# Kernel tuning notes

Measured on AMD Instinct MI355X. Metric: run time of the kernel, lower is better.

The kernel has to match this reference:

```python
import jax, jax.numpy as jnp
import numpy as np

# Config mirroring init_kwargs
B, N, DM = 16, 512, 512          # batch, max_ast_len, hidden_size
PAR_HEADS, BRO_HEADS = 4, 4
H = PAR_HEADS + BRO_HEADS        # 8 heads
DK = DM // H                     # 64
R = 8                            # max_rel_pos
L = 2                            # num_layers
DFF = 4 * DM
EPS = 1e-5


def setup_inputs() -> dict:
    key = jax.random.key(0)
    ks = jax.random.split(key, 24)
    s = 0.02
    inp = {
        "src_emb": jax.random.normal(ks[0], (B, N, DM), jnp.float32),
        "par_edges": jax.random.randint(ks[1], (B, R, N), 0, N, jnp.int32),
        "bro_edges": jax.random.randint(ks[2], (B, R, N), 0, N, jnp.int32),
        # relative-position embedding tables (par heads ++ bro heads along head axis,
        # exactly what concat_vec(rel_par_*, rel_bro_*, dim=1) produces): [H, R, DK]
        "rel_q": s * jax.random.normal(ks[3], (H, R, DK), jnp.float32),
        "rel_k": s * jax.random.normal(ks[4], (H, R, DK), jnp.float32),
        "rel_v": s * jax.random.normal(ks[5], (H, R, DK), jnp.float32),
        # per-layer weights, stacked over layers
        "Wq": s * jax.random.normal(ks[6], (L, DM, DM), jnp.float32),
        "Wk": s * jax.random.normal(ks[7], (L, DM, DM), jnp.float32),
        "Wv": s * jax.random.normal(ks[8], (L, DM, DM), jnp.float32),
        "Wo": s * jax.random.normal(ks[9], (L, DM, DM), jnp.float32),
        "ln1_g": jnp.ones((L, DM), jnp.float32),
        "ln1_b": jnp.zeros((L, DM), jnp.float32),
        "W1": s * jax.random.normal(ks[10], (L, DM, DFF), jnp.float32),
        "b1": jnp.zeros((L, DFF), jnp.float32),
        "W2": s * jax.random.normal(ks[11], (L, DFF, DM), jnp.float32),
        "b2": jnp.zeros((L, DM), jnp.float32),
        "ln2_g": jnp.ones((L, DM), jnp.float32),
        "ln2_b": jnp.zeros((L, DM), jnp.float32),
        "normf_g": jnp.ones((DM,), jnp.float32),
        "normf_b": jnp.zeros((DM,), jnp.float32),
    }
    return inp


def _ln(x, g, b):
    m = x.mean(-1, keepdims=True)
    v = ((x - m) ** 2).mean(-1, keepdims=True)
    return (x - m) * jax.lax.rsqrt(v + EPS) * g + b


def _gather_nodes(t, idx):
    # t: [B,H,N,DK], idx: [B,H,R,N,1] -> [B,H,R,N,DK] gathered along node axis
    t_b = jnp.broadcast_to(t[:, :, None], (B, H, R, N, DK))
    return jnp.take_along_axis(t_b, idx, axis=3)


def _forward(src_emb, rel_q, rel_k, rel_v, Wq, Wk, Wv, Wo, ln1_g, ln1_b,
             W1, b1, W2, b2, ln2_g, ln2_b, normf_g, normf_b,
             par_edges, bro_edges):
    # start_nodes = concat_pos: repeat par edges over par heads, bro over bro heads
    start = jnp.concatenate(
        [jnp.repeat(par_edges[:, None], PAR_HEADS, axis=1),
         jnp.repeat(bro_edges[:, None], BRO_HEADS, axis=1)], axis=1)  # [B,H,R,N]
    idx = start[..., None].astype(jnp.int32)  # [B,H,R,N,1]
    scale = 1.0 / np.sqrt(DK)
    x = src_emb
    for i in range(L):
        q = (x @ Wq[i]).reshape(B, N, H, DK).transpose(0, 2, 1, 3)  # bhnd
        k = (x @ Wk[i]).reshape(B, N, H, DK).transpose(0, 2, 1, 3)
        v = (x @ Wv[i]).reshape(B, N, H, DK).transpose(0, 2, 1, 3)
        k_s = _gather_nodes(k, idx)  # [B,H,R,N,DK]
        v_s = _gather_nodes(v, idx)
        # Shaw-style relational scores over the R sparse neighbors only
        scores = (jnp.einsum('bhnd,bhrnd->bhrn', q, k_s)
                  + jnp.einsum('bhnd,hrd->bhrn', q, rel_k)
                  + jnp.einsum('hrd,bhrnd->bhrn', rel_q, k_s)) * scale
        attn = jax.nn.softmax(scores, axis=2)  # softmax over relative positions
        ctx = (jnp.einsum('bhrn,bhrnd->bhnd', attn, v_s)
               + jnp.einsum('bhrn,hrd->bhnd', attn, rel_v))
        ctx = ctx.transpose(0, 2, 1, 3).reshape(B, N, DM)
        x = _ln(x + ctx @ Wo[i], ln1_g[i], ln1_b[i])
        ff = jax.nn.relu(x @ W1[i] + b1[i]) @ W2[i] + b2[i]
        x = _ln(x + ff, ln2_g[i], ln2_b[i])
    return _ln(x, normf_g, normf_b)  # final self.norm


def reference(src_emb, par_edges, bro_edges, rel_q, rel_k, rel_v,
              Wq, Wk, Wv, Wo, ln1_g, ln1_b, W1, b1, W2, b2,
              ln2_g, ln2_b, normf_g, normf_b):
    return _forward(src_emb, rel_q, rel_k, rel_v, Wq, Wk, Wv, Wo,
                    ln1_g, ln1_b, W1, b1, W2, b2, ln2_g, ln2_b,
                    normf_g, normf_b, par_edges, bro_edges)
```

## Files before the change

### kernel.cpp

```cpp
#include <hip/hip_runtime.h>
#include <hip/hip_bf16.h>


#define BB 16
#define NN 512
#define DMM 512
#define HH 8
#define DKK 64
#define RR 8
#define LL 2
#define DFFV 2048
#define PAR_HEADS 4
#define EPSV 1e-5f

typedef __bf16 bf16x8 __attribute__((ext_vector_type(8)));
typedef float f32x4 __attribute__((ext_vector_type(4)));
typedef unsigned short u16x8 __attribute__((ext_vector_type(8)));

__device__ __forceinline__ unsigned short f2bf(float f) {
    unsigned u = __float_as_uint(f);
    u += 0x7fff + ((u >> 16) & 1);
    return (unsigned short)(u >> 16);
}
__device__ __forceinline__ float bf2f(unsigned short u) {
    return __uint_as_float(((unsigned)u) << 16);
}

__global__ __launch_bounds__(256) void transpose_qkvo_kernel(
    const float* __restrict__ Wq, const float* __restrict__ Wk,
    const float* __restrict__ Wv, const float* __restrict__ Wo,
    unsigned short* __restrict__ wqkvT, unsigned short* __restrict__ woT)
{
    __shared__ float tile[32][33];
    int layer = blockIdx.z >> 2, which = blockIdx.z & 3;
    const float* s = (which == 0 ? Wq : which == 1 ? Wk : which == 2 ? Wv : Wo)
                     + (size_t)layer * DMM * DMM;
    unsigned short* d = (which < 3)
        ? wqkvT + (size_t)layer * 1536 * DMM + (size_t)which * DMM * DMM
        : woT + (size_t)layer * DMM * DMM;
    int k0 = blockIdx.y * 32, n0 = blockIdx.x * 32;
    int tx = threadIdx.x & 31, ty = threadIdx.x >> 5;
#pragma unroll
    for (int i = 0; i < 4; ++i)
        tile[ty + i * 8][tx] = s[(size_t)(k0 + ty + i * 8) * DMM + (n0 + tx)];
    __syncthreads();
#pragma unroll
    for (int i = 0; i < 4; ++i)
        d[(size_t)(n0 + ty + i * 8) * DMM + (k0 + tx)] = f2bf(tile[tx][ty + i * 8]);
}

__global__ __launch_bounds__(256) void transpose_w_kernel(
    const float* __restrict__ src, unsigned short* __restrict__ dst,
    int K, int N, size_t zStride)
{
    __shared__ float tile[32][33];
    const float* s = src + (size_t)blockIdx.z * K * N;
    unsigned short* d = dst + (size_t)blockIdx.z * zStride;
    int k0 = blockIdx.y * 32, n0 = blockIdx.x * 32;
    int tx = threadIdx.x & 31, ty = threadIdx.x >> 5;
#pragma unroll
    for (int i = 0; i < 4; ++i)
        tile[ty + i * 8][tx] = s[(size_t)(k0 + ty + i * 8) * N + (n0 + tx)];
    __syncthreads();
#pragma unroll
    for (int i = 0; i < 4; ++i)
        d[(size_t)(n0 + ty + i * 8) * K + (k0 + tx)] = f2bf(tile[tx][ty + i * 8]);
}

__global__ __launch_bounds__(256) void convert_x_kernel(
    const float* __restrict__ src, float* __restrict__ x, unsigned short* __restrict__ xb, int n4)
{
    int i = blockIdx.x * blockDim.x + threadIdx.x;
    int stride = gridDim.x * blockDim.x;
    for (; i < n4; i += stride) {
        float4 f = ((const float4*)src)[i];
        ((float4*)x)[i] = f;
        ushort4 u;
        u.x = f2bf(f.x); u.y = f2bf(f.y); u.z = f2bf(f.z); u.w = f2bf(f.w);
        ((ushort4*)xb)[i] = u;
    }
}

template<bool OUTBF, bool DORELU>
__global__ __launch_bounds__(256) void gemm_kernel(
    const unsigned short* __restrict__ A,
    const unsigned short* __restrict__ Bt,
    float* __restrict__ Cf,
    unsigned short* __restrict__ Cb,
    const float* __restrict__ bias,
    int M, int N, int K, int kLen)
{
    constexpr int BM = 128, BN = 64, BK = 32;
    __shared__ __align__(16) unsigned short As[2][BM * BK];
    __shared__ __align__(16) unsigned short Bs[2][BN * BK];
    int tid = threadIdx.x, lane = tid & 63, w = tid >> 6;
    int wr = w >> 1, wc = w & 1;

    int gx = gridDim.x;
    int nwg = gx * gridDim.y;
    int flat = blockIdx.x + gx * blockIdx.y;
    int qq = nwg >> 3;
    int swz = (flat & 7) * qq + (flat >> 3);
    int bx = swz % gx, by = swz / gx;
    int mBase = by * BM, nBase = bx * BN;
    int kStart = blockIdx.z * kLen;

    const unsigned short* gA = A + (size_t)mBase * K;
    const unsigned short* gB = Bt + (size_t)nBase * K;

    f32x4 acc[4][2];
#pragma unroll
    for (int i = 0; i < 4; ++i)
#pragma unroll
        for (int j = 0; j < 2; ++j) acc[i][j] = (f32x4){0.f, 0.f, 0.f, 0.f};

    auto stage = [&](int buf, int k0) {
#pragma unroll
        for (int it = 0; it < 2; ++it) {
            int i = it * 256 + tid;
            int row = i >> 2, slot = i & 3;
            int gcol = (slot ^ ((row >> 1) & 3)) * 8;
            __builtin_amdgcn_global_load_lds(
                (const __attribute__((address_space(1))) void*)(gA + (size_t)row * K + k0 + gcol),
                (__attribute__((address_space(3))) void*)(As[buf] + i * 8), 16, 0, 0);
        }
        {
            int i = tid;
            int row = i >> 2, slot = i & 3;
            int gcol = (slot ^ ((row >> 1) & 3)) * 8;
            __builtin_amdgcn_global_load_lds(
                (const __attribute__((address_space(1))) void*)(gB + (size_t)row * K + k0 + gcol),
                (__attribute__((address_space(3))) void*)(Bs[buf] + i * 8), 16, 0, 0);
        }
    };

    int nt = kLen / BK;
    stage(0, kStart);
    int cur = 0;
    for (int t = 0; t < nt; ++t) {
        if (t + 1 < nt) {
            stage(cur ^ 1, kStart + (t + 1) * BK);
            asm volatile("s_waitcnt vmcnt(3)" ::: "memory");
        } else {
            asm volatile("s_waitcnt vmcnt(0)" ::: "memory");
        }
        __builtin_amdgcn_s_barrier();

        int rsel = lane & 15, g0 = lane >> 4;
        bf16x8 a[4], b[2];
#pragma unroll
        for (int m = 0; m < 4; ++m) {
            int row = wr * 64 + m * 16 + rsel;
            int s = g0 ^ ((row >> 1) & 3);
            a[m] = *(const bf16x8*)((const char*)As[cur] + row * 64 + s * 16);
        }
#pragma unroll
        for (int n = 0; n < 2; ++n) {
            int row = wc * 32 + n * 16 + rsel;
            int s = g0 ^ ((row >> 1) & 3);
            b[n] = *(const bf16x8*)((const char*)Bs[cur] + row * 64 + s * 16);
        }
#pragma unroll
        for (int m = 0; m < 4; ++m)
#pragma unroll
            for (int n = 0; n < 2; ++n)
                acc[m][n] = __builtin_amdgcn_mfma_f32_16x16x32_bf16(a[m], b[n], acc[m][n], 0, 0, 0);
        __builtin_amdgcn_s_barrier();
        cur ^= 1;
    }

    size_t zoff = (size_t)blockIdx.z * M * N;
    int rbase = (lane >> 4) * 4;
    int cloc = lane & 15;
#pragma unroll
    for (int m = 0; m < 4; ++m) {
#pragma unroll
        for (int n = 0; n < 2; ++n) {
            int col = nBase + wc * 32 + n * 16 + cloc;
            float bv = bias ? bias[col] : 0.0f;
#pragma unroll
            for (int j = 0; j < 4; ++j) {
                int row = mBase + wr * 64 + m * 16 + rbase + j;
                float val = acc[m][n][j] + bv;
                if (DORELU) val = fmaxf(val, 0.0f);
                if (OUTBF) Cb[zoff + (size_t)row * N + col] = f2bf(val);
                else       Cf[zoff + (size_t)row * N + col] = val;
            }
        }
    }
}

__global__ __launch_bounds__(256) void attn_kernel(
    const unsigned short* __restrict__ qkv,
    const int* __restrict__ par, const int* __restrict__ bro,
    const float* __restrict__ relq, const float* __restrict__ relk,
    const float* __restrict__ relv, unsigned short* __restrict__ cb)
{
    int f = blockIdx.x;
    int xcd = f & 7;
    int j = f >> 3;
    int b = xcd + 8 * (j & 1);
    int rem = j >> 1;
    int h = rem >> 4;
    int n0 = (rem & 15) * 32;
    int w = threadIdx.x >> 6;
    int lane = threadIdx.x & 63;
    int nw = n0 + w * 8;

    float rq[RR], rk[RR], rv[RR];
#pragma unroll
    for (int r = 0; r < RR; ++r) {
        rq[r] = relq[(h * RR + r) * DKK + lane];
        rk[r] = relk[(h * RR + r) * DKK + lane];
        rv[r] = relv[(h * RR + r) * DKK + lane];
    }
    const int* edges = (h < PAR_HEADS) ? par : bro;
    int e_all = edges[(b * RR + (lane & 7)) * NN + nw + (lane >> 3)];

    const unsigned short* qrow = qkv + (size_t)b * NN * 1536 + h * DKK;

#pragma unroll
    for (int nl = 0; nl < 8; ++nl) {
        int n = nw + nl;
        float qd = bf2f(qrow[(size_t)n * 1536 + lane]);
        float t[RR];
        int e[RR];
#pragma unroll
        for (int r = 0; r < RR; ++r) {
            int er = __builtin_amdgcn_readlane(e_all, nl * 8 + r);
            e[r] = er;
            float kd = bf2f(qkv[(size_t)(b * NN + er) * 1536 + DMM + h * DKK + lane]);
            t[r] = kd * (qd + rq[r]) + qd * rk[r];
        }
        {
            bool hb = lane & 4;
#pragma unroll
            for (int rr = 0; rr < 4; ++rr) {
                float send = hb ? t[rr] : t[rr + 4];
                float keep = hb ? t[rr + 4] : t[rr];
                t[rr] = keep + __shfl_xor(send, 4, 64);
            }
        }
        {
            bool hb = lane & 2;
#pragma unroll
            for (int rr = 0; rr < 2; ++rr) {
                float send = hb ? t[rr] : t[rr + 2];
                float keep = hb ? t[rr + 2] : t[rr];
                t[rr] = keep + __shfl_xor(send, 2, 64);
            }
        }
        {
            bool hb = lane & 1;
            float send = hb ? t[0] : t[1];
            float keep = hb ? t[1] : t[0];
            t[0] = keep + __shfl_xor(send, 1, 64);
        }
        float s = t[0];
        s += __shfl_xor(s, 8, 64);
        s += __shfl_xor(s, 16, 64);
        s += __shfl_xor(s, 32, 64);
        s *= 0.125f;
        float mx = s;
        mx = fmaxf(mx, __shfl_xor(mx, 1, 64));
        mx = fmaxf(mx, __shfl_xor(mx, 2, 64));
        mx = fmaxf(mx, __shfl_xor(mx, 4, 64));
        float ee = __expf(s - mx);
        float den = ee;
        den += __shfl_xor(den, 1, 64);
        den += __shfl_xor(den, 2, 64);
        den += __shfl_xor(den, 4, 64);
        float a = ee / den;
        float od = 0.f;
#pragma unroll
        for (int r = 0; r < RR; ++r) {
            float ar = __shfl(a, (lane & 56) | r, 64);
            float vd = bf2f(qkv[(size_t)(b * NN + e[r]) * 1536 + 2 * DMM + h * DKK + lane]);
            od = fmaf(ar, vd + rv[r], od);
        }
        cb[(size_t)(b * NN + n) * DMM + h * DKK + lane] = f2bf(od);
    }
}

__global__ __launch_bounds__(256) void ln_kernel(
    const float* __restrict__ xin, const float* __restrict__ add0,
    const float* __restrict__ add1, const float* __restrict__ bias,
    float* __restrict__ xout, unsigned short* __restrict__ xbout,
    const float* __restrict__ g, const float* __restrict__ bb)
{
    int row = blockIdx.x * 4 + (threadIdx.x >> 6);
    int lane = threadIdx.x & 63;
    int c0 = lane * 8;
    const float* xr = xin + (size_t)row * DMM + c0;
    float vals[8];
    {
        float4 v0 = *(const float4*)xr;
        float4 v1 = *(const float4*)(xr + 4);
        vals[0] = v0.x; vals[1] = v0.y; vals[2] = v0.z; vals[3] = v0.w;
        vals[4] = v1.x; vals[5] = v1.y; vals[6] = v1.z; vals[7] = v1.w;
    }
    if (add0) {
        const float* ar = add0 + (size_t)row * DMM + c0;
        float4 v0 = *(const float4*)ar, v1 = *(const float4*)(ar + 4);
        vals[0] += v0.x; vals[1] += v0.y; vals[2] += v0.z; vals[3] += v0.w;
        vals[4] += v1.x; vals[5] += v1.y; vals[6] += v1.z; vals[7] += v1.w;
    }
    if (add1) {
        const float* ar = add1 + (size_t)row * DMM + c0;
        float4 v0 = *(const float4*)ar, v1 = *(const float4*)(ar + 4);
        vals[0] += v0.x; vals[1] += v0.y; vals[2] += v0.z; vals[3] += v0.w;
        vals[4] += v1.x; vals[5] += v1.y; vals[6] += v1.z; vals[7] += v1.w;
    }
    if (bias) {
        float4 v0 = *(const float4*)(bias + c0), v1 = *(const float4*)(bias + c0 + 4);
        vals[0] += v0.x; vals[1] += v0.y; vals[2] += v0.z; vals[3] += v0.w;
        vals[4] += v1.x; vals[5] += v1.y; vals[6] += v1.z; vals[7] += v1.w;
    }
    float s = 0.f;
#pragma unroll
    for (int j = 0; j < 8; ++j) s += vals[j];
#pragma unroll
    for (int off = 32; off > 0; off >>= 1) s += __shfl_xor(s, off, 64);
    float mean = s * (1.0f / DMM);
    float s2 = 0.f;
#pragma unroll
    for (int j = 0; j < 8; ++j) { float d = vals[j] - mean; s2 += d * d; }
#pragma unroll
    for (int off = 32; off > 0; off >>= 1) s2 += __shfl_xor(s2, off, 64);
    float inv = rsqrtf(s2 * (1.0f / DMM) + EPSV);

    float4 gv0 = *(const float4*)(g + c0), gv1 = *(const float4*)(g + c0 + 4);
    float4 bv0 = *(const float4*)(bb + c0), bv1 = *(const float4*)(bb + c0 + 4);
    float y[8];
    y[0] = (vals[0] - mean) * inv * gv0.x + bv0.x;
    y[1] = (vals[1] - mean) * inv * gv0.y + bv0.y;
    y[2] = (vals[2] - mean) * inv * gv0.z + bv0.z;
    y[3] = (vals[3] - mean) * inv * gv0.w + bv0.w;
    y[4] = (vals[4] - mean) * inv * gv1.x + bv1.x;
    y[5] = (vals[5] - mean) * inv * gv1.y + bv1.y;
    y[6] = (vals[6] - mean) * inv * gv1.z + bv1.z;
    y[7] = (vals[7] - mean) * inv * gv1.w + bv1.w;

    float* xo = xout + (size_t)row * DMM + c0;
    *(float4*)xo = make_float4(y[0], y[1], y[2], y[3]);
    *(float4*)(xo + 4) = make_float4(y[4], y[5], y[6], y[7]);
    if (xbout) {
        u16x8 u;
#pragma unroll
        for (int j = 0; j < 8; ++j) u[j] = f2bf(y[j]);
        *(u16x8*)(xbout + (size_t)row * DMM + c0) = u;
    }
}

extern "C" void kernel_launch(void* const* d_in, const int* in_sizes, int n_in,
                              void* d_out, int out_size, void* d_ws, size_t ws_size,
                              hipStream_t stream)
{
    const float* src_emb = (const float*)d_in[0];
    const int*   par     = (const int*)d_in[1];
    const int*   bro     = (const int*)d_in[2];
    const float* rel_q   = (const float*)d_in[3];
    const float* rel_k   = (const float*)d_in[4];
    const float* rel_v   = (const float*)d_in[5];
    const float* Wq      = (const float*)d_in[6];
    const float* Wk      = (const float*)d_in[7];
    const float* Wv      = (const float*)d_in[8];
    const float* Wo      = (const float*)d_in[9];
    const float* ln1_g   = (const float*)d_in[10];
    const float* ln1_b   = (const float*)d_in[11];
    const float* W1      = (const float*)d_in[12];
    const float* b1      = (const float*)d_in[13];
    const float* W2      = (const float*)d_in[14];
    const float* b2      = (const float*)d_in[15];
    const float* ln2_g   = (const float*)d_in[16];
    const float* ln2_b   = (const float*)d_in[17];
    const float* normf_g = (const float*)d_in[18];
    const float* normf_b = (const float*)d_in[19];

    const size_t MB = 1024 * 1024;
    const int M = BB * NN;
    char* ws = (char*)d_ws;
    float*          p    = (float*)(ws + 0 * MB);
    unsigned short* qkvb = (unsigned short*)(ws + 0 * MB);
    unsigned short* h1   = (unsigned short*)(ws + 32 * MB);
    unsigned short* xb   = (unsigned short*)(ws + 64 * MB);
    unsigned short* cbuf = (unsigned short*)(ws + 72 * MB);
    unsigned short* wqkvT = (unsigned short*)(ws + 80 * MB);
    unsigned short* woT  = wqkvT + (size_t)LL * 1536 * DMM;
    unsigned short* w1T  = woT + (size_t)LL * DMM * DMM;
    unsigned short* w2T  = w1T + (size_t)LL * DMM * DFFV;
    float* p0 = p;
    float* p1 = p + (size_t)M * DMM;
    float* x = (float*)d_out;

    transpose_qkvo_kernel<<<dim3(16, 16, LL * 4), 256, 0, stream>>>(
        Wq, Wk, Wv, Wo, wqkvT, woT);
    transpose_w_kernel<<<dim3(DFFV / 32, DMM / 32, LL), 256, 0, stream>>>(
        W1, w1T, DMM, DFFV, (size_t)DMM * DFFV);
    transpose_w_kernel<<<dim3(DMM / 32, DFFV / 32, LL), 256, 0, stream>>>(
        W2, w2T, DFFV, DMM, (size_t)DMM * DFFV);

    convert_x_kernel<<<2048, 256, 0, stream>>>(src_emb, x, xb, M * DMM / 4);

    for (int l = 0; l < LL; ++l) {
        const unsigned short* wqkv_l = wqkvT + (size_t)l * 1536 * DMM;
        const unsigned short* wo_l = woT + (size_t)l * DMM * DMM;
        const unsigned short* w1_l = w1T + (size_t)l * DMM * DFFV;
        const unsigned short* w2_l = w2T + (size_t)l * DFFV * DMM;

        gemm_kernel<true, false><<<dim3(1536 / 64, M / 128, 1), 256, 0, stream>>>(
            xb, wqkv_l, nullptr, qkvb, nullptr, M, 1536, DMM, DMM);

        attn_kernel<<<2048, 256, 0, stream>>>(qkvb, par, bro, rel_q, rel_k, rel_v, cbuf);

        gemm_kernel<false, false><<<dim3(512 / 64, M / 128, 2), 256, 0, stream>>>(
            cbuf, wo_l, p, nullptr, nullptr, M, DMM, DMM, DMM / 2);
        ln_kernel<<<M / 4, 256, 0, stream>>>(x, p0, p1, nullptr, x, xb,
                                             ln1_g + l * DMM, ln1_b + l * DMM);

        gemm_kernel<true, true><<<dim3(DFFV / 64, M / 128, 1), 256, 0, stream>>>(
            xb, w1_l, nullptr, h1, b1 + l * DFFV, M, DFFV, DMM, DMM);
        gemm_kernel<false, false><<<dim3(512 / 64, M / 128, 2), 256, 0, stream>>>(
            h1, w2_l, p, nullptr, nullptr, M, DMM, DFFV, DFFV / 2);
        ln_kernel<<<M / 4, 256, 0, stream>>>(x, p0, p1, b2 + l * DMM, x, xb,
                                             ln2_g + l * DMM, ln2_b + l * DMM);
    }

    ln_kernel<<<M / 4, 256, 0, stream>>>(x, nullptr, nullptr, nullptr, x, nullptr,
                                         normf_g, normf_b);
}
```

Baseline: 470.0 us.

## Replace double-buffered BK=32 GEMM pipeline with single-buffer BK=64 loop

```diff
diff --git a/kernel.cpp b/kernel.cpp
--- a/kernel.cpp
+++ b/kernel.cpp
@@ -90,9 +90,9 @@
     const float* __restrict__ bias,
     int M, int N, int K, int kLen)
 {
-    constexpr int BM = 128, BN = 64, BK = 32;
-    __shared__ __align__(16) unsigned short As[2][BM * BK];
-    __shared__ __align__(16) unsigned short Bs[2][BN * BK];
+    constexpr int BM = 128, BN = 64, BK = 64;
+    __shared__ __align__(16) unsigned short As[BM * BK];
+    __shared__ __align__(16) unsigned short Bs[BN * BK];
     int tid = threadIdx.x, lane = tid & 63, w = tid >> 6;
     int wr = w >> 1, wc = w & 1;
 
@@ -105,68 +105,63 @@
     int mBase = by * BM, nBase = bx * BN;
     int kStart = blockIdx.z * kLen;
 
-    const unsigned short* gA = A + (size_t)mBase * K;
-    const unsigned short* gB = Bt + (size_t)nBase * K;
-
     f32x4 acc[4][2];
 #pragma unroll
     for (int i = 0; i < 4; ++i)
 #pragma unroll
         for (int j = 0; j < 2; ++j) acc[i][j] = (f32x4){0.f, 0.f, 0.f, 0.f};
 
-    auto stage = [&](int buf, int k0) {
+    for (int k0 = kStart; k0 < kStart + kLen; k0 += BK) {
+#pragma unroll
+        for (int it = 0; it < 4; ++it) {
+            int i = it * 256 + tid;
+            int row = i >> 3, slot = i & 7;
+            int gcol = (slot ^ (row & 7)) * 8;
+            const unsigned short* ga = A + (size_t)(mBase + row) * K + k0 + gcol;
+            __builtin_amdgcn_global_load_lds(
+                (const __attribute__((address_space(1))) void*)ga,
+                (__attribute__((address_space(3))) void*)(As + i * 8), 16, 0, 0);
+        }
 #pragma unroll
         for (int it = 0; it < 2; ++it) {
             int i = it * 256 + tid;
-            int row = i >> 2, slot = i & 3;
-            int gcol = (slot ^ ((row >> 1) & 3)) * 8;
+            int row = i >> 3, slot = i & 7;
+            int gcol = (slot ^ (row & 7)) * 8;
+            const unsigned short* gb = Bt + (size_t)(nBase + row) * K + k0 + gcol;
             __builtin_amdgcn_global_load_lds(
-                (const __attribute__((address_space(1))) void*)(gA + (size_t)row * K + k0 + gcol),
-                (__attribute__((address_space(3))) void*)(As[buf] + i * 8), 16, 0, 0);
-        }
-        {
-            int i = tid;
-            int row = i >> 2, slot = i & 3;
-            int gcol = (slot ^ ((row >> 1) & 3)) * 8;
-            __builtin_amdgcn_global_load_lds(
-                (const __attribute__((address_space(1))) void*)(gB + (size_t)row * K + k0 + gcol),
-                (__attribute__((address_space(3))) void*)(Bs[buf] + i * 8), 16, 0, 0);
-        }
-    };
-
-    int nt = kLen / BK;
-    stage(0, kStart);
-    int cur = 0;
-    for (int t = 0; t < nt; ++t) {
-        if (t + 1 < nt) {
-            stage(cur ^ 1, kStart + (t + 1) * BK);
-            asm volatile("s_waitcnt vmcnt(3)" ::: "memory");
-        } else {
-            asm volatile("s_waitcnt vmcnt(0)" ::: "memory");
-        }
-        __builtin_amdgcn_s_barrier();
+                (const __attribute__((address_space(1))) void*)gb,
+                (__attribute__((address_space(3))) void*)(Bs + i * 8), 16, 0, 0);
+        }
+        __syncthreads();
 
         int rsel = lane & 15, g0 = lane >> 4;
-        bf16x8 a[4], b[2];
+        bf16x8 a[4][2], b[2][2];
 #pragma unroll
         for (int m = 0; m < 4; ++m) {
             int row = wr * 64 + m * 16 + rsel;
-            int s = g0 ^ ((row >> 1) & 3);
-            a[m] = *(const bf16x8*)((const char*)As[cur] + row * 64 + s * 16);
+#pragma unroll
+            for (int ks = 0; ks < 2; ++ks) {
+                int s = (g0 + ks * 4) ^ (row & 7);
+                a[m][ks] = *(const bf16x8*)((const char*)As + row * 128 + s * 16);
+            }
         }
 #pragma unroll
         for (int n = 0; n < 2; ++n) {
             int row = wc * 32 + n * 16 + rsel;
-            int s = g0 ^ ((row >> 1) & 3);
-            b[n] = *(const bf16x8*)((const char*)Bs[cur] + row * 64 + s * 16);
+#pragma unroll
+            for (int ks = 0; ks < 2; ++ks) {
+                int s = (g0 + ks * 4) ^ (row & 7);
+                b[n][ks] = *(const bf16x8*)((const char*)Bs + row * 128 + s * 16);
+            }
         }
 #pragma unroll
         for (int m = 0; m < 4; ++m)
 #pragma unroll
             for (int n = 0; n < 2; ++n)
-                acc[m][n] = __builtin_amdgcn_mfma_f32_16x16x32_bf16(a[m], b[n], acc[m][n], 0, 0, 0);
-        __builtin_amdgcn_s_barrier();
-        cur ^= 1;
+#pragma unroll
+                for (int ks = 0; ks < 2; ++ks)
+                    acc[m][n] = __builtin_amdgcn_mfma_f32_16x16x32_bf16(a[m][ks], b[n][ks], acc[m][n], 0, 0, 0);
+        __syncthreads();
     }
 
     size_t zoff = (size_t)blockIdx.z * M * N;
```

Result: faster. 457.2 us (-2.7%).
